# Optimization experiments

Measured on AMD Instinct MI355X. Metric: run time of the kernel, lower is better.

Reference implementation:

```python
import jax, jax.numpy as jnp
import numpy as np

B, N, K, S = 4, 50000, 128, 256  # batch, correspondences, num_subsets, num_samples
EPS = 1e-5


def setup_inputs() -> dict:
    key = jax.random.key(0)
    k1, k2, k3, k4 = jax.random.split(key, 4)
    src = jax.random.normal(k1, (B, N, 3), jnp.float32)
    tgt = jax.random.normal(k2, (B, N, 3), jnp.float32)
    w = jax.random.uniform(k3, (B, N), jnp.float32)
    sel = jax.random.randint(k4, (K, S), 0, N)
    return {"src_corr_points": src, "tgt_corr_points": tgt,
            "corr_weights": w, "sel_indices": sel}


def weighted_procrustes(src, tgt, w):
    """src,tgt: (M,S,3); w: (M,S) -> (M,4,4) rigid transforms (Kabsch/Umeyama)."""
    w = w / (jnp.sum(w, axis=1, keepdims=True) + EPS)
    w3 = w[..., None]  # (M,S,1)
    src_c = jnp.sum(src * w3, axis=1, keepdims=True)  # (M,1,3)
    tgt_c = jnp.sum(tgt * w3, axis=1, keepdims=True)
    src0 = src - src_c
    tgt0 = tgt - tgt_c
    H = jnp.einsum('msi,msj->mij', src0, w3 * tgt0)  # (M,3,3)
    Uu, _, Vh = jnp.linalg.svd(H)
    V = jnp.swapaxes(Vh, -1, -2)
    Ut = jnp.swapaxes(Uu, -1, -2)
    det = jnp.linalg.det(jnp.matmul(V, Ut))
    d = jnp.stack([jnp.ones_like(det), jnp.ones_like(det), jnp.sign(det)], axis=-1)
    R = jnp.matmul(V * d[:, None, :], Ut)  # (M,3,3)
    t = tgt_c[:, 0, :] - jnp.einsum('mij,mj->mi', R, src_c[:, 0, :])  # (M,3)
    M = R.shape[0]
    T = jnp.zeros((M, 4, 4), R.dtype)
    T = T.at[:, :3, :3].set(R).at[:, :3, 3].set(t).at[:, 3, 3].set(1.0)
    return T


def reference(src_corr_points, tgt_corr_points, corr_weights, sel_indices):
    b, n = corr_weights.shape
    k, s = sel_indices.shape
    # random-subset gather -> (b*k, s, 3) / (b*k, s)
    sel_src = src_corr_points[:, sel_indices, :].reshape(b * k, s, 3)
    sel_tgt = tgt_corr_points[:, sel_indices, :].reshape(b * k, s, 3)
    sel_w = corr_weights[:, sel_indices].reshape(b * k, s)
    transforms = weighted_procrustes(sel_src, sel_tgt, sel_w)  # (b*k,4,4)
    Tb = transforms.reshape(b, k, 4, 4)
    R = Tb[:, :, :3, :3]  # (b,k,3,3)
    t = Tb[:, :, :3, 3]   # (b,k,3)
    # apply all k hypotheses to all n src points: (b,k,n,3)
    aligned = jnp.einsum('bkij,bnj->bkni', R, src_corr_points) + t[:, :, None, :]
    diff = aligned - tgt_corr_points[:, None, :, :]
    corr_errors = jnp.linalg.norm(diff, axis=-1)  # (b,k,n)
    weighted_errors = jnp.mean(corr_errors * corr_weights[:, None, :], axis=2)  # (b,k)
    best = jnp.argmin(weighted_errors, axis=1)  # (b,)
    best_transform = Tb[jnp.arange(b), best]  # (b,4,4)
    return best_transform
```

## Files before the change

kernel.cpp:

```cpp
#include <hip/hip_runtime.h>
#include <hip/hip_bf16.h>

constexpr int B = 4;
constexpr int N = 50000;
constexpr int K = 128;
constexpr int S = 256;
constexpr int NCH = (N + 255) / 256;
constexpr float EPS = 1e-5f;

__device__ __forceinline__ float frcp  (float x) { return __builtin_amdgcn_rcpf(x); }
__device__ __forceinline__ float frsq  (float x) { return __builtin_amdgcn_rsqf(x); }
__device__ __forceinline__ float fsqrt_(float x) { return __builtin_amdgcn_sqrtf(x); }

template<int P, int Q>
__device__ __forceinline__ void rot(float (&A)[4][4], float (&V)[4][4])
{
  const float apq = A[P][Q];
  const float theta = 0.5f * (A[Q][Q] - A[P][P]) * frcp(apq);
  const float tt = copysignf(
      frcp(fabsf(theta) + fsqrt_(fmaf(theta, theta, 1.f))), theta);
  float c  = frsq(fmaf(tt, tt, 1.f));
  float sn = tt * c;
  const bool tiny = fabsf(apq) < 1e-20f;
  c  = tiny ? 1.f : c;
  sn = tiny ? 0.f : sn;
  #pragma unroll
  for (int i = 0; i < 4; ++i) {
    const float aip = A[i][P], aiq = A[i][Q];
    A[i][P] = c * aip - sn * aiq;
    A[i][Q] = sn * aip + c * aiq;
  }
  #pragma unroll
  for (int i = 0; i < 4; ++i) {
    const float api = A[P][i], aqi = A[Q][i];
    A[P][i] = c * api - sn * aqi;
    A[Q][i] = sn * api + c * aqi;
  }
  #pragma unroll
  for (int i = 0; i < 4; ++i) {
    const float vip = V[i][P], viq = V[i][Q];
    V[i][P] = c * vip - sn * viq;
    V[i][Q] = sn * vip + c * viq;
  }
}

__device__ __forceinline__ void solve_and_write(const float (&Sm)[16], float* To)
{
  const float W   = Sm[0];
  const float inv = frcp(W + EPS);
  const float scx = Sm[1]*inv, scy = Sm[2]*inv, scz = Sm[3]*inv;
  const float tcx = Sm[4]*inv, tcy = Sm[5]*inv, tcz = Sm[6]*inv;
  const float f = 2.f - W * inv;
  const float Sxx = Sm[7]*inv  - f*scx*tcx;
  const float Sxy = Sm[8]*inv  - f*scx*tcy;
  const float Sxz = Sm[9]*inv  - f*scx*tcz;
  const float Syx = Sm[10]*inv - f*scy*tcx;
  const float Syy = Sm[11]*inv - f*scy*tcy;
  const float Syz = Sm[12]*inv - f*scy*tcz;
  const float Szx = Sm[13]*inv - f*scz*tcx;
  const float Szy = Sm[14]*inv - f*scz*tcy;
  const float Szz = Sm[15]*inv - f*scz*tcz;

  float A[4][4], V[4][4];
  A[0][0] = Sxx + Syy + Szz;
  A[0][1] = Syz - Szy;  A[0][2] = Szx - Sxz;  A[0][3] = Sxy - Syx;
  A[1][1] = Sxx - Syy - Szz;
  A[1][2] = Sxy + Syx;  A[1][3] = Szx + Sxz;
  A[2][2] = -Sxx + Syy - Szz;
  A[2][3] = Syz + Szy;
  A[3][3] = -Sxx - Syy + Szz;
  A[1][0] = A[0][1]; A[2][0] = A[0][2]; A[3][0] = A[0][3];
  A[2][1] = A[1][2]; A[3][1] = A[1][3]; A[3][2] = A[2][3];

  #pragma unroll
  for (int i = 0; i < 4; ++i)
    #pragma unroll
    for (int j = 0; j < 4; ++j) V[i][j] = (i == j) ? 1.f : 0.f;

  #pragma unroll 1
  for (int sweep = 0; sweep < 5; ++sweep) {
    rot<0,1>(A, V); rot<0,2>(A, V); rot<0,3>(A, V);
    rot<1,2>(A, V); rot<1,3>(A, V); rot<2,3>(A, V);
  }

  const float d0 = A[0][0], d1 = A[1][1], d2 = A[2][2], d3 = A[3][3];
  const bool b1 = d1 > d0;
  const bool b3 = d3 > d2;
  const bool bb = (b3 ? d3 : d2) > (b1 ? d1 : d0);
  float qw  = bb ? (b3 ? V[0][3] : V[0][2]) : (b1 ? V[0][1] : V[0][0]);
  float qxv = bb ? (b3 ? V[1][3] : V[1][2]) : (b1 ? V[1][1] : V[1][0]);
  float qyv = bb ? (b3 ? V[2][3] : V[2][2]) : (b1 ? V[2][1] : V[2][0]);
  float qzv = bb ? (b3 ? V[3][3] : V[3][2]) : (b1 ? V[3][1] : V[3][0]);

  const float qn = frsq(qw*qw + qxv*qxv + qyv*qyv + qzv*qzv);
  qw *= qn; qxv *= qn; qyv *= qn; qzv *= qn;

  const float R00 = 1.f - 2.f*(qyv*qyv + qzv*qzv);
  const float R01 = 2.f*(qxv*qyv - qw*qzv);
  const float R02 = 2.f*(qxv*qzv + qw*qyv);
  const float R10 = 2.f*(qxv*qyv + qw*qzv);
  const float R11 = 1.f - 2.f*(qxv*qxv + qzv*qzv);
  const float R12 = 2.f*(qyv*qzv - qw*qxv);
  const float R20 = 2.f*(qxv*qzv - qw*qyv);
  const float R21 = 2.f*(qyv*qzv + qw*qxv);
  const float R22 = 1.f - 2.f*(qxv*qxv + qyv*qyv);

  const float tx = tcx - (R00*scx + R01*scy + R02*scz);
  const float ty = tcy - (R10*scx + R11*scy + R12*scz);
  const float tz = tcz - (R20*scx + R21*scy + R22*scz);

  float4* T4 = (float4*)To;
  T4[0] = make_float4(R00, R01, R02, tx);
  T4[1] = make_float4(R10, R11, R12, ty);
  T4[2] = make_float4(R20, R21, R22, tz);
  T4[3] = make_float4(0.f, 0.f, 0.f, 1.f);
}

__global__ __launch_bounds__(256) void pack_kernel(
    const float* __restrict__ src, const float* __restrict__ tgt,
    const float* __restrict__ wts, float4* __restrict__ packed)
{
  const int n = blockIdx.x * 256 + threadIdx.x;
  if (n >= N) return;
  float4 rec[8];
  #pragma unroll
  for (int b = 0; b < B; ++b) {
    const int i = b * N + n;
    rec[b*2]   = make_float4(src[3*i], src[3*i+1], src[3*i+2], wts[i]);
    rec[b*2+1] = make_float4(tgt[3*i], tgt[3*i+1], tgt[3*i+2], 0.f);
  }
  float4* out = packed + (size_t)n * 8;
  #pragma unroll
  for (int r = 0; r < 8; ++r) out[r] = rec[r];
}

template<bool PACKED>
__global__ __launch_bounds__(1024) void gather_solve_kernel(
    const float4* __restrict__ packed,
    const float* __restrict__ src, const float* __restrict__ tgt,
    const float* __restrict__ wts, const int* __restrict__ sel,
    float* __restrict__ T)
{
  const int k   = blockIdx.x;
  const int tid = threadIdx.x;
  const int s   = tid >> 2;
  const int b   = tid & 3;

  const int idx = sel[k * S + s];

  float px, py, pz, qx, qy, qz, w;
  if (PACKED) {
    const float4 P = packed[(size_t)idx * 8 + b * 2];
    const float4 Q = packed[(size_t)idx * 8 + b * 2 + 1];
    px = P.x; py = P.y; pz = P.z; w = P.w;
    qx = Q.x; qy = Q.y; qz = Q.z;
  } else {
    const float* ps = src + (size_t)(b * N + idx) * 3;
    const float* pt = tgt + (size_t)(b * N + idx) * 3;
    w  = wts[b * N + idx];
    px = ps[0]; py = ps[1]; pz = ps[2];
    qx = pt[0]; qy = pt[1]; qz = pt[2];
  }

  float acc[16];
  acc[0] = w;
  acc[1] = w * px;  acc[2] = w * py;  acc[3] = w * pz;
  acc[4] = w * qx;  acc[5] = w * qy;  acc[6] = w * qz;
  acc[7]  = w * px * qx; acc[8]  = w * px * qy; acc[9]  = w * px * qz;
  acc[10] = w * py * qx; acc[11] = w * py * qy; acc[12] = w * py * qz;
  acc[13] = w * pz * qx; acc[14] = w * pz * qy; acc[15] = w * pz * qz;

  #pragma unroll
  for (int off = 32; off >= 4; off >>= 1) {
    #pragma unroll
    for (int i = 0; i < 16; ++i)
      acc[i] += __shfl_down(acc[i], off);
  }

  __shared__ float red[16][4][16];
  __shared__ float SmS[4][17];
  const int lane = tid & 63, wv = tid >> 6;
  if (lane < 4) {
    #pragma unroll
    for (int i = 0; i < 16; ++i) red[wv][lane][i] = acc[i];
  }
  __syncthreads();

  if (tid < 64) {
    const int bb = tid >> 4, m = tid & 15;
    float t = 0.f;
    #pragma unroll
    for (int wgi = 0; wgi < 16; ++wgi) t += red[wgi][bb][m];
    SmS[bb][m] = t;
  }
  __syncthreads();

  if (tid < 4) {
    float Sm[16];
    #pragma unroll
    for (int z = 0; z < 16; ++z) Sm[z] = SmS[tid][z];
    solve_and_write(Sm, T + (size_t)(tid * K + k) * 16);
  }
}

constexpr int KPT = 4;
constexpr int KG  = K / KPT;
constexpr int NSL = 256 / KG;
constexpr int PPS = 256 / NSL;

__global__ __launch_bounds__(256) void error_kernel(
    const float* __restrict__ src, const float* __restrict__ tgt,
    const float* __restrict__ wts, const float* __restrict__ T,
    float* __restrict__ partial)
{
  __shared__ float4 sp[256];
  __shared__ float4 sq[256];
  __shared__ float  t4[K][12];
  __shared__ float  red[K][NSL + 1];

  const int blk = blockIdx.x;
  const int b   = blk / NCH;
  const int ch  = blk - b * NCH;
  const int tid = threadIdx.x;
  const int j   = ch * 256 + tid;

  float4 P = make_float4(0.f, 0.f, 0.f, 0.f);
  float4 Q = make_float4(0.f, 0.f, 0.f, 0.f);
  if (j < N) {
    const float* ps = src + (size_t)(b*N + j) * 3;
    const float* pt = tgt + (size_t)(b*N + j) * 3;
    P.x = ps[0]; P.y = ps[1]; P.z = ps[2]; P.w = wts[b*N + j];
    Q.x = pt[0]; Q.y = pt[1]; Q.z = pt[2];
  }
  sp[tid] = P; sq[tid] = Q;

  if (tid < K) {
    const float* tp = T + (size_t)(b*K + tid) * 16;
    #pragma unroll
    for (int c = 0; c < 12; ++c) t4[tid][c] = tp[c];
  }
  __syncthreads();

  const int kg    = tid & (KG - 1);
  const int slice = tid >> 5;

  float R[KPT][12];
  #pragma unroll
  for (int m = 0; m < KPT; ++m) {
    const int k = kg + m * KG;
    #pragma unroll
    for (int c = 0; c < 12; ++c) R[m][c] = t4[k][c];
  }

  float acc[KPT] = {0.f, 0.f, 0.f, 0.f};
  const int base = slice * PPS;
  #pragma unroll 4
  for (int i = 0; i < PPS; ++i) {
    const float4 p = sp[base + i];
    const float4 q = sq[base + i];
    #pragma unroll
    for (int m = 0; m < KPT; ++m) {
      const float dx = fmaf(R[m][0], p.x, fmaf(R[m][1], p.y, fmaf(R[m][2],  p.z, R[m][3])))  - q.x;
      const float dy = fmaf(R[m][4], p.x, fmaf(R[m][5], p.y, fmaf(R[m][6],  p.z, R[m][7])))  - q.y;
      const float dz = fmaf(R[m][8], p.x, fmaf(R[m][9], p.y, fmaf(R[m][10], p.z, R[m][11]))) - q.z;
      const float d2 = fmaf(dx, dx, fmaf(dy, dy, dz*dz));
      acc[m] = fmaf(p.w, fsqrt_(d2), acc[m]);
    }
  }

  #pragma unroll
  for (int m = 0; m < KPT; ++m)
    red[kg + m * KG][slice] = acc[m];
  __syncthreads();

  if (tid < K) {
    float sum = 0.f;
    #pragma unroll
    for (int s2 = 0; s2 < NSL; ++s2) sum += red[tid][s2];
    partial[((size_t)b * NCH + ch) * K + tid] = sum;
  }
}

__global__ __launch_bounds__(256) void argmin_kernel(
    const float* __restrict__ partial, const float* __restrict__ T,
    float* __restrict__ out)
{
  const int b   = blockIdx.x;
  const int tid = threadIdx.x;
  const int k   = tid & (K - 1);
  const int h   = tid >> 7;

  float sum = 0.f;
  #pragma unroll 7
  for (int c = h; c < NCH; c += 2)
    sum += partial[((size_t)b * NCH + c) * K + k];

  __shared__ float vals[256];
  __shared__ int   idxs[K];
  vals[tid] = sum;
  __syncthreads();

  if (tid < K) { vals[tid] = vals[tid] + vals[tid + K]; idxs[tid] = tid; }
  __syncthreads();

  for (int off = K / 2; off > 0; off >>= 1) {
    if (tid < off) {
      const float o = vals[tid + off];
      if (o < vals[tid] || (o == vals[tid] && idxs[tid + off] < idxs[tid])) {
        vals[tid] = o; idxs[tid] = idxs[tid + off];
      }
    }
    __syncthreads();
  }

  const int best = idxs[0];
  if (tid < 16) out[(size_t)b * 16 + tid] = T[(size_t)(b * K + best) * 16 + tid];
}

extern "C" void kernel_launch(void* const* d_in, const int* in_sizes, int n_in,
                              void* d_out, int out_size, void* d_ws, size_t ws_size,
                              hipStream_t stream) {
  const float* src = (const float*)d_in[0];
  const float* tgt = (const float*)d_in[1];
  const float* wts = (const float*)d_in[2];
  const int*   sel = (const int*)d_in[3];

  const size_t packed_bytes   = (size_t)N * 8 * sizeof(float4);
  const size_t T_floats       = (size_t)B * K * 16;
  const size_t partial_floats = (size_t)B * NCH * K;
  const bool fast = ws_size >=
      packed_bytes + (T_floats + partial_floats) * sizeof(float);

  if (fast) {
    float4* packed  = (float4*)d_ws;
    float*  T       = (float*)((char*)d_ws + packed_bytes);
    float*  partial = T + T_floats;

    pack_kernel<<<(N + 255) / 256, 256, 0, stream>>>(src, tgt, wts, packed);
    gather_solve_kernel<true><<<K, 1024, 0, stream>>>(
        packed, src, tgt, wts, sel, T);
    error_kernel<<<B * NCH, 256, 0, stream>>>(src, tgt, wts, T, partial);
    argmin_kernel<<<B, 256, 0, stream>>>(partial, T, (float*)d_out);
  } else {
    float* T       = (float*)d_ws;
    float* partial = T + T_floats;

    gather_solve_kernel<false><<<K, 1024, 0, stream>>>(
        nullptr, src, tgt, wts, sel, T);
    error_kernel<<<B * NCH, 256, 0, stream>>>(src, tgt, wts, T, partial);
    argmin_kernel<<<B, 256, 0, stream>>>(partial, T, (float*)d_out);
  }
}
```

Measured before the change: 43.75 us.

## Drop pack kernel and gather directly with XCD-aware per-batch solve blocks

Removes the pack kernel that rewrote all points into an interleaved float4 layout, so the full input is no longer read and rewritten each call. The gather-solve kernel now launches one 256-thread block per (batch, subset) and maps block ids so each XCD handles one batch, aiming to keep that batch's gathered data in its local L2. The final reduction becomes a full-wave shuffle plus a 4-way shared-memory sum. The trade-off is uncoalesced strided scalar gathers from the original arrays and four times as many blocks.

```diff
diff --git a/kernel.cpp b/kernel.cpp
--- a/kernel.cpp
+++ b/kernel.cpp
@@ -116,51 +116,23 @@
   T4[3] = make_float4(0.f, 0.f, 0.f, 1.f);
 }
 
-__global__ __launch_bounds__(256) void pack_kernel(
-    const float* __restrict__ src, const float* __restrict__ tgt,
-    const float* __restrict__ wts, float4* __restrict__ packed)
-{
-  const int n = blockIdx.x * 256 + threadIdx.x;
-  if (n >= N) return;
-  float4 rec[8];
-  #pragma unroll
-  for (int b = 0; b < B; ++b) {
-    const int i = b * N + n;
-    rec[b*2]   = make_float4(src[3*i], src[3*i+1], src[3*i+2], wts[i]);
-    rec[b*2+1] = make_float4(tgt[3*i], tgt[3*i+1], tgt[3*i+2], 0.f);
-  }
-  float4* out = packed + (size_t)n * 8;
-  #pragma unroll
-  for (int r = 0; r < 8; ++r) out[r] = rec[r];
-}
-
-template<bool PACKED>
-__global__ __launch_bounds__(1024) void gather_solve_kernel(
-    const float4* __restrict__ packed,
+__global__ __launch_bounds__(256) void gather_solve_kernel(
     const float* __restrict__ src, const float* __restrict__ tgt,
     const float* __restrict__ wts, const int* __restrict__ sel,
     float* __restrict__ T)
 {
-  const int k   = blockIdx.x;
-  const int tid = threadIdx.x;
-  const int s   = tid >> 2;
-  const int b   = tid & 3;
+  const int bid = blockIdx.x;
+  const int xcd = bid & 7;
+  const int b   = xcd >> 1;
+  const int k   = ((bid >> 3) << 1) | (xcd & 1);
+  const int s   = threadIdx.x;
 
   const int idx = sel[k * S + s];
-
-  float px, py, pz, qx, qy, qz, w;
-  if (PACKED) {
-    const float4 P = packed[(size_t)idx * 8 + b * 2];
-    const float4 Q = packed[(size_t)idx * 8 + b * 2 + 1];
-    px = P.x; py = P.y; pz = P.z; w = P.w;
-    qx = Q.x; qy = Q.y; qz = Q.z;
-  } else {
-    const float* ps = src + (size_t)(b * N + idx) * 3;
-    const float* pt = tgt + (size_t)(b * N + idx) * 3;
-    w  = wts[b * N + idx];
-    px = ps[0]; py = ps[1]; pz = ps[2];
-    qx = pt[0]; qy = pt[1]; qz = pt[2];
-  }
+  const float* ps = src + (size_t)(b * N + idx) * 3;
+  const float* pt = tgt + (size_t)(b * N + idx) * 3;
+  const float w  = wts[b * N + idx];
+  const float px = ps[0], py = ps[1], pz = ps[2];
+  const float qx = pt[0], qy = pt[1], qz = pt[2];
 
   float acc[16];
   acc[0] = w;
@@ -171,35 +143,26 @@
   acc[13] = w * pz * qx; acc[14] = w * pz * qy; acc[15] = w * pz * qz;
 
   #pragma unroll
-  for (int off = 32; off >= 4; off >>= 1) {
+  for (int off = 32; off > 0; off >>= 1) {
     #pragma unroll
     for (int i = 0; i < 16; ++i)
       acc[i] += __shfl_down(acc[i], off);
   }
 
-  __shared__ float red[16][4][16];
-  __shared__ float SmS[4][17];
-  const int lane = tid & 63, wv = tid >> 6;
-  if (lane < 4) {
-    #pragma unroll
-    for (int i = 0; i < 16; ++i) red[wv][lane][i] = acc[i];
-  }
-  __syncthreads();
-
-  if (tid < 64) {
-    const int bb = tid >> 4, m = tid & 15;
-    float t = 0.f;
-    #pragma unroll
-    for (int wgi = 0; wgi < 16; ++wgi) t += red[wgi][bb][m];
-    SmS[bb][m] = t;
-  }
-  __syncthreads();
-
-  if (tid < 4) {
+  __shared__ float red[4][16];
+  const int lane = threadIdx.x & 63, wv = threadIdx.x >> 6;
+  if (lane == 0) {
+    #pragma unroll
+    for (int i = 0; i < 16; ++i) red[wv][i] = acc[i];
+  }
+  __syncthreads();
+
+  if (threadIdx.x == 0) {
     float Sm[16];
     #pragma unroll
-    for (int z = 0; z < 16; ++z) Sm[z] = SmS[tid][z];
-    solve_and_write(Sm, T + (size_t)(tid * K + k) * 16);
+    for (int i = 0; i < 16; ++i)
+      Sm[i] = red[0][i] + red[1][i] + red[2][i] + red[3][i];
+    solve_and_write(Sm, T + (size_t)(b * K + k) * 16);
   }
 }
 
@@ -325,29 +288,10 @@
   const float* wts = (const float*)d_in[2];
   const int*   sel = (const int*)d_in[3];
 
-  const size_t packed_bytes   = (size_t)N * 8 * sizeof(float4);
-  const size_t T_floats       = (size_t)B * K * 16;
-  const size_t partial_floats = (size_t)B * NCH * K;
-  const bool fast = ws_size >=
-      packed_bytes + (T_floats + partial_floats) * sizeof(float);
-
-  if (fast) {
-    float4* packed  = (float4*)d_ws;
-    float*  T       = (float*)((char*)d_ws + packed_bytes);
-    float*  partial = T + T_floats;
-
-    pack_kernel<<<(N + 255) / 256, 256, 0, stream>>>(src, tgt, wts, packed);
-    gather_solve_kernel<true><<<K, 1024, 0, stream>>>(
-        packed, src, tgt, wts, sel, T);
-    error_kernel<<<B * NCH, 256, 0, stream>>>(src, tgt, wts, T, partial);
-    argmin_kernel<<<B, 256, 0, stream>>>(partial, T, (float*)d_out);
-  } else {
-    float* T       = (float*)d_ws;
-    float* partial = T + T_floats;
-
-    gather_solve_kernel<false><<<K, 1024, 0, stream>>>(
-        nullptr, src, tgt, wts, sel, T);
-    error_kernel<<<B * NCH, 256, 0, stream>>>(src, tgt, wts, T, partial);
-    argmin_kernel<<<B, 256, 0, stream>>>(partial, T, (float*)d_out);
-  }
-}
+  float* T       = (float*)d_ws;
+  float* partial = T + (size_t)B * K * 16;
+
+  gather_solve_kernel<<<B * K, 256, 0, stream>>>(src, tgt, wts, sel, T);
+  error_kernel<<<B * NCH, 256, 0, stream>>>(src, tgt, wts, T, partial);
+  argmin_kernel<<<B, 256, 0, stream>>>(partial, T, (float*)d_out);
+}
```

Measured after the change: 43.58 us. No clear change (-0.4%).
